# Kernel tuning notes

Measured on AMD Instinct MI355X. Metric: run time of the kernel, lower is better.

## Reference

```python
import jax, jax.numpy as jnp
import numpy as np

# ---- LSS config (grid_conf / data_aug_conf) ----
XB = (-50.0, 50.0, 0.5); YB = (-50.0, 50.0, 0.5)
ZB = (-10.0, 10.0, 20.0); DB = (4.0, 45.0, 1.0)
OGFH, OGFW = 128, 352
DS = 16
FH, FW = OGFH // DS, OGFW // DS            # 8, 22
DNUM = int((DB[1] - DB[0]) / DB[2])        # 41 depth bins
CAMC = 64
B, N = 8, 6
NXX, NXY, NXZ = 200, 200, 1
K = NXX * NXY * NXZ

DX = jnp.array([XB[2], YB[2], ZB[2]], jnp.float32)
BX = jnp.array([XB[0] + XB[2] / 2.0, YB[0] + YB[2] / 2.0, ZB[0] + ZB[2] / 2.0], jnp.float32)
NX = jnp.array([NXX, NXY, NXZ], jnp.int32)


def create_frustum():
    ds = np.arange(DB[0], DB[1], DB[2], dtype=np.float32).reshape(-1, 1, 1) * np.ones((1, FH, FW), np.float32)
    xs = np.linspace(0, OGFW - 1, FW, dtype=np.float32).reshape(1, 1, FW) * np.ones((DNUM, FH, 1), np.float32)
    ys = np.linspace(0, OGFH - 1, FH, dtype=np.float32).reshape(1, FH, 1) * np.ones((DNUM, 1, FW), np.float32)
    return jnp.asarray(np.stack([xs, ys, ds], -1))  # [D, fH, fW, 3]

FRUSTUM = create_frustum()


def safe_inverse_3x3(M, eps=1e-8):
    a, b, c = M[..., 0, 0], M[..., 0, 1], M[..., 0, 2]
    d, e, f = M[..., 1, 0], M[..., 1, 1], M[..., 1, 2]
    g, h, i = M[..., 2, 0], M[..., 2, 1], M[..., 2, 2]
    A = e * i - f * h; Bc = -(d * i - f * g); Cc = d * h - e * g
    Dc = -(b * i - c * h); E = a * i - c * g; F = -(a * h - b * g)
    G = b * f - c * e; H = -(a * f - c * d); I = a * e - b * d
    det = jnp.maximum(a * A + b * Bc + c * Cc, eps)
    inv = jnp.stack([jnp.stack([A, Dc, G], -1),
                     jnp.stack([Bc, E, H], -1),
                     jnp.stack([Cc, F, I], -1)], -2)
    return inv / det[..., None, None]


def get_geometry(rots, trans, intrins, post_rots, post_trans):
    # frustum: [D, fH, fW, 3] -> [B, N, D, fH, fW, 3] in ego frame
    points = FRUSTUM[None, None] - post_trans[:, :, None, None, None]
    points = jnp.einsum('bnij,bndhwj->bndhwi', safe_inverse_3x3(post_rots), points)
    points = jnp.concatenate([points[..., :2] * points[..., 2:3], points[..., 2:3]], axis=-1)
    combine = jnp.einsum('bnij,bnjk->bnik', rots, safe_inverse_3x3(intrins))
    points = jnp.einsum('bnij,bndhwj->bndhwi', combine, points)
    return points + trans[:, :, None, None, None]


def voxel_pooling(geom, x):
    # geom: [B,N,D,H,W,3], x: [B,N,D,H,W,C]
    Nprime = B * N * DNUM * FH * FW
    xf = x.reshape(Nprime, CAMC)
    # torch .long() truncates toward zero; astype int32 matches
    gi = ((geom - (BX - DX / 2.0)) / DX).astype(jnp.int32).reshape(Nprime, 3)
    batch_ix = jnp.repeat(jnp.arange(B, dtype=jnp.int32), Nprime // B)
    kept = jnp.all((gi >= 0) & (gi < NX[None, :]), axis=1)
    ranks = batch_ix * K + gi[:, 2] * (NXX * NXY) + gi[:, 0] * NXY + gi[:, 1]
    ranks = jnp.where(kept, ranks, B * K)  # dump invalid points into a trash segment
    pooled = jax.ops.segment_sum(xf, ranks, num_segments=B * K + 1)[:B * K]  # [B*K, C]
    final = pooled.reshape(B, NXZ, NXX, NXY, CAMC).transpose(0, 4, 1, 2, 3)
    return final.reshape(B, CAMC * NXZ, NXX, NXY)  # cat over z (nz=1)


def setup_inputs() -> dict:
    key = jax.random.key(0)
    ks = jax.random.split(key, 6)
    cam_out = jax.random.normal(ks[0], (B * N, DNUM + CAMC, FH, FW), jnp.float32)
    # camera->ego rotation: cam (x right, y down, z fwd) -> ego (x fwd, y left, z up)
    R = jnp.array([[0.0, 0.0, 1.0], [-1.0, 0.0, 0.0], [0.0, -1.0, 0.0]], jnp.float32)
    rots = R + 0.02 * jax.random.normal(ks[1], (B, N, 3, 3), jnp.float32)
    trans = jnp.concatenate([
        2.0 * jax.random.normal(ks[2], (B, N, 2), jnp.float32),
        1.5 + 0.1 * jax.random.normal(jax.random.fold_in(ks[2], 1), (B, N, 1), jnp.float32)], axis=-1)
    intr = jnp.array([[260.0, 0.0, OGFW / 2.0], [0.0, 260.0, OGFH / 2.0], [0.0, 0.0, 1.0]], jnp.float32)
    scale = jnp.array([[5.0, 0.0, 5.0], [0.0, 5.0, 5.0], [0.0, 0.0, 0.0]], jnp.float32)
    intrins = intr + scale * jax.random.normal(ks[3], (B, N, 3, 3), jnp.float32)
    post_rots = jnp.eye(3, dtype=jnp.float32) + 0.01 * jax.random.normal(ks[4], (B, N, 3, 3), jnp.float32)
    post_trans = 2.0 * jax.random.normal(ks[5], (B, N, 3), jnp.float32)
    return {"cam_out": cam_out, "rots": rots, "trans": trans, "intrins": intrins,
            "post_rots": post_rots, "post_trans": post_trans}


def reference(cam_out, rots, trans, intrins, post_rots, post_trans):
    geom = get_geometry(rots, trans, intrins, post_rots, post_trans)
    # lift: depth distribution x context features (outer product)
    depth = jax.nn.softmax(cam_out[:, :DNUM], axis=1)          # [BN, D, fH, fW]
    feats = cam_out[:, DNUM:DNUM + CAMC]                       # [BN, C, fH, fW]
    new_x = depth[:, None] * feats[:, :, None]                 # [BN, C, D, fH, fW]
    x = new_x.reshape(B, N, CAMC, DNUM, FH, FW).transpose(0, 1, 3, 4, 5, 2)  # [B,N,D,H,W,C]
    return voxel_pooling(geom, x)                              # [B, C, 200, 200]
```

## Files before the change

### kernel.cpp

```cpp
#include <hip/hip_runtime.h>
#include <math.h>

#define DNUM 41
#define FH 8
#define FW 22
#define CAMC 64
#define NB 8
#define NCAM 6
#define BN 48
#define NXX 200
#define NXY 200
#define KVOX 40000
#define CAM_CH (DNUM + CAMC)
#define HW (FH * FW)
#define CAM_STRIDE (CAM_CH * HW)
#define OUT_PER_B (CAMC * KVOX)
#define SCRATCH_FLOATS ((size_t)NB * KVOX * CAMC)
#define NXCD 8

__device__ __forceinline__ void inv3x3(const float* __restrict__ m, float* __restrict__ o) {
  #pragma clang fp contract(off)
  float a=m[0], b=m[1], c=m[2];
  float d=m[3], e=m[4], f=m[5];
  float g=m[6], h=m[7], i=m[8];
  float A  =  e*i - f*h;
  float Bc = -(d*i - f*g);
  float Cc =  d*h - e*g;
  float Dc = -(b*i - c*h);
  float E  =  a*i - c*g;
  float F  = -(a*h - b*g);
  float G  =  b*f - c*e;
  float H  = -(a*f - c*d);
  float I  =  a*e - b*d;
  float det = fmaxf((a*A + b*Bc) + c*Cc, 1e-8f);
  o[0]=A/det;  o[1]=Dc/det; o[2]=G/det;
  o[3]=Bc/det; o[4]=E/det;  o[5]=H/det;
  o[6]=Cc/det; o[7]=F/det;  o[8]=I/det;
}

__global__ __launch_bounds__(256) void lss_zero(float4* __restrict__ ws4) {
  const int id = blockIdx.x;
  const int b  = id & 7;
  const int j  = id >> 3;
  const float4 z = make_float4(0.f, 0.f, 0.f, 0.f);
  float4* p = ws4 + (size_t)b*(OUT_PER_B/4) + (size_t)j*1024 + threadIdx.x;
  p[0] = z; p[256] = z; p[512] = z; p[768] = z;
}

__global__ __launch_bounds__(512) void lss_scatter_col(const float* __restrict__ cam_out,
                                                       const float* __restrict__ rots,
                                                       const float* __restrict__ trans,
                                                       const float* __restrict__ intrins,
                                                       const float* __restrict__ post_rots,
                                                       const float* __restrict__ post_trans,
                                                       float* __restrict__ dst) {
  #pragma clang fp contract(off)
  const int blk  = blockIdx.x;
  const int b    = blk & 7;
  const int j    = blk >> 3;
  const int bn   = b*NCAM + (j / FW);
  const int w    = j - (j / FW)*FW;
  const int tid  = threadIdx.x;
  const int wv   = tid >> 6;
  const int lane = tid & 63;

  __shared__ float sP[9], sM[9], sPT[3], sTR[3];
  __shared__ float sDep[FH][DNUM + 1];
  __shared__ int   sVox[FH][DNUM + 1];
  __shared__ float sFeat[FH][CAMC];

  if (tid == 0) {
    float P[9], IC[9], M[9];
    inv3x3(post_rots + bn*9, P);
    inv3x3(intrins + bn*9, IC);
    const float* R = rots + bn*9;
    #pragma unroll
    for (int r = 0; r < 3; r++)
      #pragma unroll
      for (int k = 0; k < 3; k++)
        M[r*3+k] = (R[r*3+0]*IC[0+k] + R[r*3+1]*IC[3+k]) + R[r*3+2]*IC[6+k];
    #pragma unroll
    for (int q = 0; q < 9; q++) { sP[q] = P[q]; sM[q] = M[q]; }
  } else if (tid >= 8 && tid < 11) {
    sPT[tid-8]  = post_trans[bn*3 + (tid-8)];
  } else if (tid >= 11 && tid < 14) {
    sTR[tid-11] = trans[bn*3 + (tid-11)];
  }

  const int colbase = bn*CAM_STRIDE + w;

  {
    int fh = tid >> 6, c = tid & 63;
    sFeat[fh][c] = cam_out[colbase + (DNUM + c)*HW + fh*FW];
  }
  __syncthreads();

  const float fx = (float)((double)w * (351.0 / 21.0));

  {
    const int h = wv;
    float logit = (lane < DNUM) ? cam_out[colbase + lane*HW + h*FW] : -INFINITY;
    float mx = logit;
    #pragma unroll
    for (int off = 32; off >= 1; off >>= 1) mx = fmaxf(mx, __shfl_xor(mx, off, 64));
    float e = expf(logit - mx);
    float s = e;
    #pragma unroll
    for (int off = 32; off >= 1; off >>= 1) s += __shfl_xor(s, off, 64);
    if (lane < DNUM) {
      float fy = (float)((double)h * (127.0 / 7.0));
      float fz = 4.0f + (float)lane;
      float p0 = fx - sPT[0], p1 = fy - sPT[1], p2 = fz - sPT[2];
      float q0 = (sP[0]*p0 + sP[1]*p1) + sP[2]*p2;
      float q1 = (sP[3]*p0 + sP[4]*p1) + sP[5]*p2;
      float q2 = (sP[6]*p0 + sP[7]*p1) + sP[8]*p2;
      float r0 = q0*q2, r1 = q1*q2, r2 = q2;
      float g0 = ((sM[0]*r0 + sM[1]*r1) + sM[2]*r2) + sTR[0];
      float g1 = ((sM[3]*r0 + sM[4]*r1) + sM[5]*r2) + sTR[1];
      float g2 = ((sM[6]*r0 + sM[7]*r1) + sM[8]*r2) + sTR[2];
      int ix = (int)((g0 + 50.0f) / 0.5f);
      int iy = (int)((g1 + 50.0f) / 0.5f);
      int iz = (int)((g2 + 10.0f) / 20.0f);
      bool kept = (ix >= 0) & (ix < NXX) & (iy >= 0) & (iy < NXY) & (iz == 0);
      sVox[h][lane] = kept ? (ix*NXY + iy) : -1;
      sDep[h][lane] = e / s;
    }
  }
  __syncthreads();

  float* __restrict__ sb = dst + (size_t)b*OUT_PER_B + lane;
  for (int d = wv; d < DNUM; d += 8) {
    unsigned done = 0;
    #pragma unroll
    for (int h = 0; h < FH; h++) {
      if ((done >> h) & 1u) continue;
      int v = sVox[h][d];
      if (v < 0) continue;
      float wsum = sDep[h][d] * sFeat[h][lane];
      #pragma unroll
      for (int h2 = h + 1; h2 < FH; h2++) {
        if (sVox[h2][d] == v) {
          wsum += sDep[h2][d] * sFeat[h2][lane];
          done |= 1u << h2;
        }
      }
      atomicAdd(sb + (size_t)v*CAMC, wsum);
    }
  }
}

__global__ __launch_bounds__(256) void lss_transpose(const float* __restrict__ src,
                                                     float* __restrict__ out) {
  __shared__ float tile[64][65];
  const int id = blockIdx.x;
  const int b  = id & 7;
  const int v0 = (id >> 3) * 64;
  const int tx = threadIdx.x & 63;
  const int ty = threadIdx.x >> 6;
  const float* s = src + ((size_t)b*KVOX + v0) * CAMC;
  #pragma unroll
  for (int r = ty; r < 64; r += 4)
    tile[r][tx] = s[r*CAMC + tx];
  __syncthreads();
  float* dstp = out + (size_t)b*OUT_PER_B + v0;
  #pragma unroll
  for (int r = ty; r < 64; r += 4)
    dstp[(size_t)r*KVOX + tx] = tile[tx][r];
}

__global__ void lss_prep(const float* __restrict__ rots,
                         const float* __restrict__ intrins,
                         const float* __restrict__ post_rots,
                         float* __restrict__ prep) {
  #pragma clang fp contract(off)
  int bn = threadIdx.x;
  if (bn >= BN) return;
  float P[9], IC[9];
  inv3x3(post_rots + bn*9, P);
  inv3x3(intrins + bn*9, IC);
  const float* R = rots + bn*9;
  float* o = prep + bn*18;
  #pragma unroll
  for (int q = 0; q < 9; q++) o[q] = P[q];
  #pragma unroll
  for (int r = 0; r < 3; r++)
    #pragma unroll
    for (int k = 0; k < 3; k++)
      o[9 + r*3 + k] = (R[r*3+0]*IC[0+k] + R[r*3+1]*IC[3+k]) + R[r*3+2]*IC[6+k];
}

__global__ __launch_bounds__(64) void lss_scatter_direct(const float* __restrict__ cam_out,
                                                         const float* __restrict__ trans,
                                                         const float* __restrict__ post_trans,
                                                         const float* __restrict__ prep,
                                                         float* __restrict__ out) {
  #pragma clang fp contract(off)
  const int blk = blockIdx.x;
  const int bn  = blk / HW;
  const int pix = blk % HW;
  const int h   = pix / FW;
  const int w   = pix % FW;
  const int b   = bn / NCAM;
  const int tid = threadIdx.x;
  __shared__ float sP[9], sM[9], sPT[3], sTR[3];
  __shared__ float sDepth[DNUM];
  __shared__ int   sVoff[DNUM];
  if (tid < 9)       sP[tid]      = prep[bn*18 + tid];
  else if (tid < 18) sM[tid-9]    = prep[bn*18 + tid];
  else if (tid < 21) sPT[tid-18]  = post_trans[bn*3 + (tid-18)];
  else if (tid < 24) sTR[tid-21]  = trans[bn*3 + (tid-21)];
  __syncthreads();
  const int base = bn*CAM_STRIDE + h*FW + w;
  float logit = (tid < DNUM) ? cam_out[base + tid*HW] : -INFINITY;
  float mx = logit;
  #pragma unroll
  for (int off = 32; off >= 1; off >>= 1) mx = fmaxf(mx, __shfl_xor(mx, off, 64));
  float e = expf(logit - mx);
  float s = e;
  #pragma unroll
  for (int off = 32; off >= 1; off >>= 1) s += __shfl_xor(s, off, 64);
  float depth = e / s;
  if (tid < DNUM) {
    float fx = (float)((double)w * (351.0 / 21.0));
    float fy = (float)((double)h * (127.0 / 7.0));
    float fz = 4.0f + (float)tid;
    float p0 = fx - sPT[0], p1 = fy - sPT[1], p2 = fz - sPT[2];
    float q0 = (sP[0]*p0 + sP[1]*p1) + sP[2]*p2;
    float q1 = (sP[3]*p0 + sP[4]*p1) + sP[5]*p2;
    float q2 = (sP[6]*p0 + sP[7]*p1) + sP[8]*p2;
    float r0 = q0*q2, r1 = q1*q2, r2 = q2;
    float g0 = ((sM[0]*r0 + sM[1]*r1) + sM[2]*r2) + sTR[0];
    float g1 = ((sM[3]*r0 + sM[4]*r1) + sM[5]*r2) + sTR[1];
    float g2 = ((sM[6]*r0 + sM[7]*r1) + sM[8]*r2) + sTR[2];
    int ix = (int)((g0 + 50.0f) / 0.5f);
    int iy = (int)((g1 + 50.0f) / 0.5f);
    int iz = (int)((g2 + 10.0f) / 20.0f);
    bool kept = (ix >= 0) & (ix < NXX) & (iy >= 0) & (iy < NXY) & (iz == 0);
    sVoff[tid]  = kept ? (ix*NXY + iy) : -1;
    sDepth[tid] = depth;
  }
  __syncthreads();
  const float feat = cam_out[base + (DNUM + tid)*HW];
  float* outb = out + (size_t)b*OUT_PER_B + (size_t)tid*KVOX;
  #pragma unroll 1
  for (int d = 0; d < DNUM; d++) {
    int v = sVoff[d];
    if (v >= 0) atomicAdd(outb + v, sDepth[d] * feat);
  }
}

extern "C" void kernel_launch(void* const* d_in, const int* in_sizes, int n_in,
                              void* d_out, int out_size, void* d_ws, size_t ws_size,
                              hipStream_t stream) {
  const float* cam_out    = (const float*)d_in[0];
  const float* rots       = (const float*)d_in[1];
  const float* trans      = (const float*)d_in[2];
  const float* intrins    = (const float*)d_in[3];
  const float* post_rots  = (const float*)d_in[4];
  const float* post_trans = (const float*)d_in[5];
  float* out = (float*)d_out;
  float* ws  = (float*)d_ws;

  const size_t scratch_bytes = SCRATCH_FLOATS * sizeof(float);
  const bool use_scratch = ws_size >= scratch_bytes;

  if (use_scratch) {
    lss_zero<<<5000, 256, 0, stream>>>((float4*)ws);
    lss_scatter_col<<<BN * FW, 512, 0, stream>>>(cam_out, rots, trans, intrins,
                                                 post_rots, post_trans, ws);
    lss_transpose<<<5000, 256, 0, stream>>>(ws, out);
  } else {
    float* prep = ws;
    hipMemsetAsync(out, 0, (size_t)out_size * sizeof(float), stream);
    lss_prep<<<1, 64, 0, stream>>>(rots, intrins, post_rots, prep);
    lss_scatter_direct<<<BN * HW, 64, 0, stream>>>(cam_out, trans, post_trans, prep, out);
  }
}
```

Measured before the change: 89.43 us.

## Split scatter into geometry pass and finer-grained atomic scatter kernel

The fused per-column scatter kernel becomes two kernels. The first computes voxel indices and softmax depths and writes them, with transposed features, to workspace. The second launches one wavefront per (column, depth) task and does the atomic accumulation, giving many more blocks to spread the atomic traffic across the GPU. It costs an extra launch and a global-memory round trip for records and features, and it needs a larger workspace; if the workspace is too small the code falls back to the direct path.

```diff
diff --git a/kernel.cpp b/kernel.cpp
--- a/kernel.cpp
+++ b/kernel.cpp
@@ -16,7 +16,12 @@
 #define CAM_STRIDE (CAM_CH * HW)
 #define OUT_PER_B (CAMC * KVOX)
 #define SCRATCH_FLOATS ((size_t)NB * KVOX * CAMC)
-#define NXCD 8
+#define NCPB (NCAM * FW)
+#define NCOL (NB * NCPB)
+#define PIXT (NCOL * FH)
+#define NPTS (NCOL * FH * DNUM)
+#define TASKS_PB (NCPB * DNUM)
+#define ATOM_BLKS_PB (TASKS_PB / 4)
 
 __device__ __forceinline__ void inv3x3(const float* __restrict__ m, float* __restrict__ o) {
   #pragma clang fp contract(off)
@@ -47,19 +52,21 @@
   p[0] = z; p[256] = z; p[512] = z; p[768] = z;
 }
 
-__global__ __launch_bounds__(512) void lss_scatter_col(const float* __restrict__ cam_out,
-                                                       const float* __restrict__ rots,
-                                                       const float* __restrict__ trans,
-                                                       const float* __restrict__ intrins,
-                                                       const float* __restrict__ post_rots,
-                                                       const float* __restrict__ post_trans,
-                                                       float* __restrict__ dst) {
+__global__ __launch_bounds__(512) void lss_geom(const float* __restrict__ cam_out,
+                                                const float* __restrict__ rots,
+                                                const float* __restrict__ trans,
+                                                const float* __restrict__ intrins,
+                                                const float* __restrict__ post_rots,
+                                                const float* __restrict__ post_trans,
+                                                float* __restrict__ featT,
+                                                int2* __restrict__ recs) {
   #pragma clang fp contract(off)
   const int blk  = blockIdx.x;
   const int b    = blk & 7;
   const int j    = blk >> 3;
   const int bn   = b*NCAM + (j / FW);
   const int w    = j - (j / FW)*FW;
+  const int col  = b*NCPB + j;
   const int tid  = threadIdx.x;
   const int wv   = tid >> 6;
   const int lane = tid & 63;
@@ -67,7 +74,6 @@
   __shared__ float sP[9], sM[9], sPT[3], sTR[3];
   __shared__ float sDep[FH][DNUM + 1];
   __shared__ int   sVox[FH][DNUM + 1];
-  __shared__ float sFeat[FH][CAMC];
 
   if (tid == 0) {
     float P[9], IC[9], M[9];
@@ -91,7 +97,8 @@
 
   {
     int fh = tid >> 6, c = tid & 63;
-    sFeat[fh][c] = cam_out[colbase + (DNUM + c)*HW + fh*FW];
+    float fv = cam_out[colbase + (DNUM + c)*HW + fh*FW];
+    featT[((size_t)(col*FH + fh))*CAMC + c] = fv;
   }
   __syncthreads();
 
@@ -128,24 +135,57 @@
   }
   __syncthreads();
 
+  int2* __restrict__ rc = recs + (size_t)col*DNUM*FH;
+  for (int e = tid; e < DNUM*FH; e += 512) {
+    int d = e >> 3, h = e & 7;
+    rc[e] = make_int2(sVox[h][d], __float_as_int(sDep[h][d]));
+  }
+}
+
+__global__ __launch_bounds__(256) void lss_atomic(const int2* __restrict__ recs,
+                                                  const float* __restrict__ featT,
+                                                  float* __restrict__ dst) {
+  const int blk  = blockIdx.x;
+  const int b    = blk & 7;
+  const int q    = blk >> 3;
+  const int wv   = (threadIdx.x >> 6);
+  const int lane = threadIdx.x & 63;
+  const int task = q*4 + wv;
+  const int j    = task / DNUM;
+  const int d    = task - j*DNUM;
+  const int col  = b*NCPB + j;
+
+  const int2* __restrict__ r8 = recs + ((size_t)col*DNUM + d)*FH;
+  int   vox[FH];
+  float dep[FH];
+  #pragma unroll
+  for (int h = 0; h < FH; h++) {
+    int2 e = r8[h];
+    vox[h] = e.x;
+    dep[h] = __int_as_float(e.y);
+  }
+
+  float f[FH];
+  const float* __restrict__ ft = featT + (size_t)col*FH*CAMC + lane;
+  #pragma unroll
+  for (int h = 0; h < FH; h++) f[h] = ft[h*CAMC];
+
   float* __restrict__ sb = dst + (size_t)b*OUT_PER_B + lane;
-  for (int d = wv; d < DNUM; d += 8) {
-    unsigned done = 0;
-    #pragma unroll
-    for (int h = 0; h < FH; h++) {
-      if ((done >> h) & 1u) continue;
-      int v = sVox[h][d];
-      if (v < 0) continue;
-      float wsum = sDep[h][d] * sFeat[h][lane];
-      #pragma unroll
-      for (int h2 = h + 1; h2 < FH; h2++) {
-        if (sVox[h2][d] == v) {
-          wsum += sDep[h2][d] * sFeat[h2][lane];
-          done |= 1u << h2;
-        }
+  unsigned done = 0;
+  #pragma unroll
+  for (int h = 0; h < FH; h++) {
+    if ((done >> h) & 1u) continue;
+    int v = vox[h];
+    if (v < 0) continue;
+    float wsum = dep[h] * f[h];
+    #pragma unroll
+    for (int h2 = h + 1; h2 < FH; h2++) {
+      if (vox[h2] == v) {
+        wsum += dep[h2] * f[h2];
+        done |= 1u << h2;
       }
-      atomicAdd(sb + (size_t)v*CAMC, wsum);
     }
+    atomicAdd(sb + (size_t)v*CAMC, wsum);
   }
 }
 
@@ -259,18 +299,21 @@
   const float* post_rots  = (const float*)d_in[4];
   const float* post_trans = (const float*)d_in[5];
   float* out = (float*)d_out;
-  float* ws  = (float*)d_ws;
-
-  const size_t scratch_bytes = SCRATCH_FLOATS * sizeof(float);
-  const bool use_scratch = ws_size >= scratch_bytes;
-
-  if (use_scratch) {
-    lss_zero<<<5000, 256, 0, stream>>>((float4*)ws);
-    lss_scatter_col<<<BN * FW, 512, 0, stream>>>(cam_out, rots, trans, intrins,
-                                                 post_rots, post_trans, ws);
-    lss_transpose<<<5000, 256, 0, stream>>>(ws, out);
+  char*  ws  = (char*)d_ws;
+
+  float* scratch = (float*)ws;
+  float* featT   = scratch + SCRATCH_FLOATS;
+  int2*  recs    = (int2*)(featT + (size_t)PIXT*CAMC);
+  const size_t need = SCRATCH_FLOATS*4 + (size_t)PIXT*CAMC*4 + (size_t)NPTS*8;
+
+  if (ws_size >= need) {
+    lss_zero<<<5000, 256, 0, stream>>>((float4*)scratch);
+    lss_geom<<<NCOL, 512, 0, stream>>>(cam_out, rots, trans, intrins,
+                                       post_rots, post_trans, featT, recs);
+    lss_atomic<<<ATOM_BLKS_PB * 8, 256, 0, stream>>>(recs, featT, scratch);
+    lss_transpose<<<5000, 256, 0, stream>>>(scratch, out);
   } else {
-    float* prep = ws;
+    float* prep = (float*)ws;
     hipMemsetAsync(out, 0, (size_t)out_size * sizeof(float), stream);
     lss_prep<<<1, 64, 0, stream>>>(rots, intrins, post_rots, prep);
     lss_scatter_direct<<<BN * HW, 64, 0, stream>>>(cam_out, trans, post_trans, prep, out);
```

Measured after the change: 84.81 us. -5.2%, faster.
